# Kernel optimization log

Hardware: AMD Instinct MI355X
Metric: run time of the kernel (lower is better)

The kernel has to match this reference:

```python
import jax, jax.numpy as jnp
import numpy as np

# ---- static module config (matches torch defaults) ----
N_LEVELS = 16
MIN_RES = 16
MAX_RES = 512
N_ENC = 2 ** 14
D = 3          # n_input_dims
E = 2          # n_embed_dims
B = 1 << 20    # number of query points

# per-level resolutions, computed in float32 to mirror torch's float32 log/exp
_gf = np.exp((np.log(np.float32(MAX_RES)) - np.log(np.float32(MIN_RES))) / np.float32(N_LEVELS - 1)).astype(np.float32)
RES = [int(np.floor(np.float32(MIN_RES) * _gf ** np.float32(l))) for l in range(N_LEVELS)]
DIRECT = [r ** D < N_ENC for r in RES]                  # small grids use direct ravel indexing
NLE = [min(r ** D, N_ENC) for r in RES]                  # encodings per level (sentinel row at index NLE[l])

# 2^D corner offsets, shape (8, 3)
OFFS = np.stack(np.meshgrid(*([np.arange(2)] * D), indexing='ij'), axis=-1).reshape(-1, D).astype(np.int32)
# instant-ngp spatial hashing primes
PRIMES = (1, 2654435761, 805459861)


def setup_inputs() -> dict:
    key = jax.random.key(0)
    k1, k2 = jax.random.split(key)
    x = jax.random.uniform(k1, (B, D), dtype=jnp.float32, minval=-1.0, maxval=1.0)
    # stacked per-level tables, padded to (N_ENC+1, E); rows >= NLE[l] zeroed
    emb = jax.random.uniform(k2, (N_LEVELS, N_ENC + 1, E), dtype=jnp.float32, minval=-1e-4, maxval=1e-4)
    row = np.arange(N_ENC + 1)
    valid = (row[None, :] < np.asarray(NLE)[:, None])    # (L, N_ENC+1); also zeroes the sentinel row
    emb = emb * jnp.asarray(valid[..., None], dtype=jnp.float32)
    return {"x": x, "emb": emb}


def _level_features(x, emb_l, R, n_encs, direct):
    offs = jnp.asarray(OFFS)                             # (8, 3)
    xs = (x + 1.0) * (R * 0.5) - 0.5                     # grid coords
    xl = jnp.floor(xs)
    frac = xs - xl                                       # (B, 3)
    xi = xl.astype(jnp.int32)
    c = xi[:, None, :] + offs[None, :, :]                # (B, 8, 3) corner indices
    # bilinear/trilinear weights: prod over dims of frac (offset=1) or 1-frac (offset=0)
    w = jnp.prod(jnp.where(offs[None].astype(bool), frac[:, None, :], 1.0 - frac[:, None, :]), axis=-1)  # (B, 8)
    w = jax.lax.stop_gradient(w)                         # torch computes weights under no_grad
    m = jnp.all((c >= 0) & (c < R), axis=-1)             # (B, 8) corner validity
    if direct:
        ids = (c[..., 0] * R + c[..., 1]) * R + c[..., 2]
    else:
        cu = c.astype(jnp.uint32)
        h = (cu[..., 0] * jnp.uint32(PRIMES[0])
             ^ cu[..., 1] * jnp.uint32(PRIMES[1])
             ^ cu[..., 2] * jnp.uint32(PRIMES[2]))
        ids = (h % jnp.uint32(n_encs)).astype(jnp.int32)
    ids = jnp.where(m, ids, n_encs)                      # invalid corners -> zero sentinel row
    return jnp.sum(emb_l[ids] * w[..., None], axis=1)    # (B, E)


def reference(x, emb):
    feats = [
        _level_features(x, emb[l], RES[l], NLE[l], DIRECT[l])
        for l in range(N_LEVELS)
    ]
    return jnp.stack(feats, axis=1)                      # (B, L, E)
```

## Files before the change

### kernel.cpp

```cpp
#include <hip/hip_runtime.h>
#include <hip/hip_fp16.h>


typedef __attribute__((ext_vector_type(2))) float f32x2;

#define B_POINTS (1 << 20)
#define N_LEVELS 16
#define TAB_F2   16385
#define TAB_H2   16384
#define WG       1024
#define NWG      512
#define NCHUNK   (NWG / N_LEVELS)
#define CHUNK    (B_POINTS / NCHUNK)
#define PPT      (CHUNK / WG)
#define GRP      4
#define NGRP     (PPT / GRP)

__constant__ int   cRES[N_LEVELS]  = {16, 20, 25, 32, 40, 50, 64, 80,
                                      101, 128, 161, 203, 256, 322, 406, 512};
__constant__ float cHALF[N_LEVELS] = {8.f, 10.f, 12.5f, 16.f, 20.f, 25.f, 32.f, 40.f,
                                      50.5f, 64.f, 80.5f, 101.5f, 128.f, 161.f, 203.f, 256.f};

__global__ __launch_bounds__(WG, 8)
void hashenc_lds(const float* __restrict__ x,
                 const float* __restrict__ emb,
                 float* __restrict__ out)
{
    __shared__ __half2 tab[TAB_H2];

    const int bid = blockIdx.x;
    const int xcd = bid & 7;
    const int s   = bid >> 3;
    const int l   = s & 15;
    const int c   = ((s >> 4) << 3) | xcd;

    const int   R      = cRES[l];
    const int   Rm1    = R - 1;
    const float half   = cHALF[l];
    const float hb     = half - 0.5f;
    const bool  direct = (l < 3);
    const int   R4     = R * 4;
    const int   RR4    = R * R * 4;

    const f32x2* __restrict__ gtab = (const f32x2*)emb + (size_t)l * TAB_F2;
    const int t    = threadIdx.x;
    const int base = c * CHUNK + t;

    float xa[GRP], xb[GRP], xcv[GRP];
#pragma unroll
    for (int j = 0; j < GRP; ++j) {
        const int p = base + j * WG;
        xa[j] = x[p * 3 + 0]; xb[j] = x[p * 3 + 1]; xcv[j] = x[p * 3 + 2];
    }

#pragma unroll
    for (int j = 0; j < 16; ++j) {
        const f32x2 v = gtab[j * WG + t];
        __half2 h;
        h.x = __float2half_rn(v.x);
        h.y = __float2half_rn(v.y);
        tab[j * WG + t] = h;
    }
    __syncthreads();

    const char* tb = (const char*)tab;

    for (int kg = 0; kg < NGRP; ++kg) {
        float ca[GRP], cb[GRP], cc[GRP];
#pragma unroll
        for (int j = 0; j < GRP; ++j) { ca[j] = xa[j]; cb[j] = xb[j]; cc[j] = xcv[j]; }

        if (kg + 1 < NGRP) {
#pragma unroll
            for (int j = 0; j < GRP; ++j) {
                const int p = base + (kg + 1) * (GRP * WG) + j * WG;
                xa[j] = x[p * 3 + 0]; xb[j] = x[p * 3 + 1]; xcv[j] = x[p * 3 + 2];
            }
        }

#pragma unroll
        for (int j = 0; j < GRP; ++j) {
            const int p = base + kg * (GRP * WG) + j * WG;

            const float xs0 = fmaf(ca[j], half, hb);
            const float xs1 = fmaf(cb[j], half, hb);
            const float xs2 = fmaf(cc[j], half, hb);
            const float fl0 = floorf(xs0), fl1 = floorf(xs1), fl2 = floorf(xs2);
            const float f0 = xs0 - fl0, f1 = xs1 - fl1, f2 = xs2 - fl2;
            const float g0 = 1.0f - f0, g1 = 1.0f - f1, g2 = 1.0f - f2;
            const int i0 = (int)fl0, i1 = (int)fl1, i2 = (int)fl2;

            const float wx0 = (i0 >= 0)  ? g0 : 0.0f;
            const float wx1 = (i0 < Rm1) ? f0 : 0.0f;
            const float wy0 = (i1 >= 0)  ? g1 : 0.0f;
            const float wy1 = (i1 < Rm1) ? f1 : 0.0f;
            const float wz0 = (i2 >= 0)  ? g2 : 0.0f;
            const float wz1 = (i2 < Rm1) ? f2 : 0.0f;

            const float pxy00 = wx0 * wy0, pxy01 = wx0 * wy1;
            const float pxy10 = wx1 * wy0, pxy11 = wx1 * wy1;
            const float w0 = pxy00 * wz0, w1 = pxy00 * wz1;
            const float w2 = pxy01 * wz0, w3 = pxy01 * wz1;
            const float w4 = pxy10 * wz0, w5 = pxy10 * wz1;
            const float w6 = pxy11 * wz0, w7 = pxy11 * wz1;

            unsigned d0, d1, d2, d3, d4, d5, d6, d7;
            if (direct) {
                const int u0l = max(i0, 0), u0h = min(i0 + 1, Rm1);
                const int u1l = max(i1, 0), u1h = min(i1 + 1, Rm1);
                const int u2l = max(i2, 0), u2h = min(i2 + 1, Rm1);
                const int a0  = u0l * RR4,     a1  = u0h * RR4;
                const int b00 = a0 + u1l * R4, b01 = a0 + u1h * R4;
                const int b10 = a1 + u1l * R4, b11 = a1 + u1h * R4;
                const int zl  = u2l * 4,       zh  = u2h * 4;
                d0 = b00 + zl; d1 = b00 + zh; d2 = b01 + zl; d3 = b01 + zh;
                d4 = b10 + zl; d5 = b10 + zh; d6 = b11 + zl; d7 = b11 + zh;
            } else {
                const unsigned MB  = 16383u << 2;
                const unsigned hx0 = (unsigned)i0 << 2,                 hx1 = hx0 + 4u;
                const unsigned hy0 = (unsigned)i1 * (2654435761u * 4u), hy1 = hy0 + (2654435761u * 4u);
                const unsigned hzf = (unsigned)i2 * (805459861u * 4u);
                const unsigned hz0 = hzf & MB, hz1 = (hzf + (805459861u * 4u)) & MB;
                const unsigned t00 = (hx0 ^ hy0) & MB, t01 = (hx0 ^ hy1) & MB;
                const unsigned t10 = (hx1 ^ hy0) & MB, t11 = (hx1 ^ hy1) & MB;
                d0 = t00 ^ hz0; d1 = t00 ^ hz1; d2 = t01 ^ hz0; d3 = t01 ^ hz1;
                d4 = t10 ^ hz0; d5 = t10 ^ hz1; d6 = t11 ^ hz0; d7 = t11 ^ hz1;
            }

            float acc0 = 0.0f, acc1 = 0.0f;
            {
                const __half2 e0 = *(const __half2*)(tb + d0);
                const __half2 e1 = *(const __half2*)(tb + d1);
                const __half2 e2 = *(const __half2*)(tb + d2);
                const __half2 e3 = *(const __half2*)(tb + d3);
                const __half2 e4 = *(const __half2*)(tb + d4);
                const __half2 e5 = *(const __half2*)(tb + d5);
                const __half2 e6 = *(const __half2*)(tb + d6);
                const __half2 e7 = *(const __half2*)(tb + d7);
                acc0 = fmaf(__low2float(e0),  w0, acc0); acc1 = fmaf(__high2float(e0), w0, acc1);
                acc0 = fmaf(__low2float(e1),  w1, acc0); acc1 = fmaf(__high2float(e1), w1, acc1);
                acc0 = fmaf(__low2float(e2),  w2, acc0); acc1 = fmaf(__high2float(e2), w2, acc1);
                acc0 = fmaf(__low2float(e3),  w3, acc0); acc1 = fmaf(__high2float(e3), w3, acc1);
                acc0 = fmaf(__low2float(e4),  w4, acc0); acc1 = fmaf(__high2float(e4), w4, acc1);
                acc0 = fmaf(__low2float(e5),  w5, acc0); acc1 = fmaf(__high2float(e5), w5, acc1);
                acc0 = fmaf(__low2float(e6),  w6, acc0); acc1 = fmaf(__high2float(e6), w6, acc1);
                acc0 = fmaf(__low2float(e7),  w7, acc0); acc1 = fmaf(__high2float(e7), w7, acc1);
            }

            ((float2*)out)[(size_t)p * N_LEVELS + l] = make_float2(acc0, acc1);
        }
    }
}

extern "C" void kernel_launch(void* const* d_in, const int* in_sizes, int n_in,
                              void* d_out, int out_size, void* d_ws, size_t ws_size,
                              hipStream_t stream) {
    const float* x   = (const float*)d_in[0];
    const float* emb = (const float*)d_in[1];
    float* out = (float*)d_out;

    hashenc_lds<<<NWG, WG, 0, stream>>>(x, emb, out);
}
```

Before: 209.7 us.

## Process two levels per workgroup with a combined 128KB LDS table

Each workgroup now stages the half-precision tables of two adjacent levels into a 128KB shared buffer, with the small direct-indexed levels packed tightly. It computes both levels for every point. This halves the number of workgroups and x reloads, and lets each point write a 16-byte float4 instead of two 8-byte stores. Coordinate loads are also switched to float3 vector loads. In exchange, LDS use per workgroup doubles, which lowers occupancy to fewer resident workgroups per CU, and each workgroup does more work over a longer run.

```diff
diff --git a/kernel.cpp b/kernel.cpp
--- a/kernel.cpp
+++ b/kernel.cpp
@@ -7,10 +7,10 @@
 #define B_POINTS (1 << 20)
 #define N_LEVELS 16
 #define TAB_F2   16385
-#define TAB_H2   16384
 #define WG       1024
-#define NWG      512
-#define NCHUNK   (NWG / N_LEVELS)
+#define NWG      256
+#define NPAIR    8
+#define NCHUNK   (NWG / NPAIR)
 #define CHUNK    (B_POINTS / NCHUNK)
 #define PPT      (CHUNK / WG)
 #define GRP      4
@@ -20,47 +20,142 @@
                                       101, 128, 161, 203, 256, 322, 406, 512};
 __constant__ float cHALF[N_LEVELS] = {8.f, 10.f, 12.5f, 16.f, 20.f, 25.f, 32.f, 40.f,
                                       50.5f, 64.f, 80.5f, 101.5f, 128.f, 161.f, 203.f, 256.f};
+__constant__ int   cROWS[N_LEVELS] = {4096, 8000, 15625, 16384, 16384, 16384, 16384, 16384,
+                                      16384, 16384, 16384, 16384, 16384, 16384, 16384, 16384};
+__constant__ int   cBASE[N_LEVELS] = {0, 4096, 16384, 0, 0, 16384, 0, 16384,
+                                      0, 16384, 0, 16384, 0, 16384, 0, 16384};
 
-__global__ __launch_bounds__(WG, 8)
-void hashenc_lds(const float* __restrict__ x,
-                 const float* __restrict__ emb,
-                 float* __restrict__ out)
+__device__ __forceinline__ void level_feat(const char* __restrict__ tb,
+                                           float cx, float cy, float cz,
+                                           int R, int Rm1, float half, float hb,
+                                           bool direct, unsigned base4,
+                                           float& acc0, float& acc1)
 {
-    __shared__ __half2 tab[TAB_H2];
+    const float xs0 = fmaf(cx, half, hb);
+    const float xs1 = fmaf(cy, half, hb);
+    const float xs2 = fmaf(cz, half, hb);
+    const float fl0 = floorf(xs0), fl1 = floorf(xs1), fl2 = floorf(xs2);
+    const float f0 = xs0 - fl0, f1 = xs1 - fl1, f2 = xs2 - fl2;
+    const float g0 = 1.0f - f0, g1 = 1.0f - f1, g2 = 1.0f - f2;
+    const int i0 = (int)fl0, i1 = (int)fl1, i2 = (int)fl2;
+
+    const float wx0 = (i0 >= 0)  ? g0 : 0.0f;
+    const float wx1 = (i0 < Rm1) ? f0 : 0.0f;
+    const float wy0 = (i1 >= 0)  ? g1 : 0.0f;
+    const float wy1 = (i1 < Rm1) ? f1 : 0.0f;
+    const float wz0 = (i2 >= 0)  ? g2 : 0.0f;
+    const float wz1 = (i2 < Rm1) ? f2 : 0.0f;
+
+    const float pxy00 = wx0 * wy0, pxy01 = wx0 * wy1;
+    const float pxy10 = wx1 * wy0, pxy11 = wx1 * wy1;
+    const float w0 = pxy00 * wz0, w1 = pxy00 * wz1;
+    const float w2 = pxy01 * wz0, w3 = pxy01 * wz1;
+    const float w4 = pxy10 * wz0, w5 = pxy10 * wz1;
+    const float w6 = pxy11 * wz0, w7 = pxy11 * wz1;
+
+    unsigned d0, d1, d2, d3, d4, d5, d6, d7;
+    if (direct) {
+        const int R4  = R * 4;
+        const int RR4 = R * R * 4;
+        const int u0l = max(i0, 0), u0h = min(i0 + 1, Rm1);
+        const int u1l = max(i1, 0), u1h = min(i1 + 1, Rm1);
+        const int u2l = max(i2, 0), u2h = min(i2 + 1, Rm1);
+        const int a0  = u0l * RR4 + (int)base4, a1 = u0h * RR4 + (int)base4;
+        const int b00 = a0 + u1l * R4, b01 = a0 + u1h * R4;
+        const int b10 = a1 + u1l * R4, b11 = a1 + u1h * R4;
+        const int zl  = u2l * 4,       zh  = u2h * 4;
+        d0 = b00 + zl; d1 = b00 + zh; d2 = b01 + zl; d3 = b01 + zh;
+        d4 = b10 + zl; d5 = b10 + zh; d6 = b11 + zl; d7 = b11 + zh;
+    } else {
+        const unsigned MB  = 16383u << 2;
+        const unsigned hx0 = (unsigned)i0 << 2,                 hx1 = hx0 + 4u;
+        const unsigned hy0 = (unsigned)i1 * (2654435761u * 4u), hy1 = hy0 + (2654435761u * 4u);
+        const unsigned hzf = (unsigned)i2 * (805459861u * 4u);
+        const unsigned hz0 = (hzf & MB) | base4;
+        const unsigned hz1 = ((hzf + (805459861u * 4u)) & MB) | base4;
+        const unsigned t00 = (hx0 ^ hy0) & MB, t01 = (hx0 ^ hy1) & MB;
+        const unsigned t10 = (hx1 ^ hy0) & MB, t11 = (hx1 ^ hy1) & MB;
+        d0 = t00 ^ hz0; d1 = t00 ^ hz1; d2 = t01 ^ hz0; d3 = t01 ^ hz1;
+        d4 = t10 ^ hz0; d5 = t10 ^ hz1; d6 = t11 ^ hz0; d7 = t11 ^ hz1;
+    }
+
+    const __half2 e0 = *(const __half2*)(tb + d0);
+    const __half2 e1 = *(const __half2*)(tb + d1);
+    const __half2 e2 = *(const __half2*)(tb + d2);
+    const __half2 e3 = *(const __half2*)(tb + d3);
+    const __half2 e4 = *(const __half2*)(tb + d4);
+    const __half2 e5 = *(const __half2*)(tb + d5);
+    const __half2 e6 = *(const __half2*)(tb + d6);
+    const __half2 e7 = *(const __half2*)(tb + d7);
+    acc0 = 0.0f; acc1 = 0.0f;
+    acc0 = fmaf(__low2float(e0),  w0, acc0); acc1 = fmaf(__high2float(e0), w0, acc1);
+    acc0 = fmaf(__low2float(e1),  w1, acc0); acc1 = fmaf(__high2float(e1), w1, acc1);
+    acc0 = fmaf(__low2float(e2),  w2, acc0); acc1 = fmaf(__high2float(e2), w2, acc1);
+    acc0 = fmaf(__low2float(e3),  w3, acc0); acc1 = fmaf(__high2float(e3), w3, acc1);
+    acc0 = fmaf(__low2float(e4),  w4, acc0); acc1 = fmaf(__high2float(e4), w4, acc1);
+    acc0 = fmaf(__low2float(e5),  w5, acc0); acc1 = fmaf(__high2float(e5), w5, acc1);
+    acc0 = fmaf(__low2float(e6),  w6, acc0); acc1 = fmaf(__high2float(e6), w6, acc1);
+    acc0 = fmaf(__low2float(e7),  w7, acc0); acc1 = fmaf(__high2float(e7), w7, acc1);
+}
+
+__device__ __forceinline__ void stage_level(__half2* __restrict__ tab,
+                                            const f32x2* __restrict__ src,
+                                            int rows, int obase, int t)
+{
+    for (int r0 = 0; r0 < rows; r0 += 4 * WG) {
+        f32x2 v[4];
+#pragma unroll
+        for (int u = 0; u < 4; ++u) {
+            const int r = r0 + u * WG + t;
+            if (r < rows) v[u] = src[r];
+        }
+#pragma unroll
+        for (int u = 0; u < 4; ++u) {
+            const int r = r0 + u * WG + t;
+            if (r < rows) {
+                __half2 h;
+                h.x = __float2half_rn(v[u].x);
+                h.y = __float2half_rn(v[u].y);
+                tab[obase + r] = h;
+            }
+        }
+    }
+}
+
+__global__ __launch_bounds__(WG, 4)
+void hashenc_pair(const float* __restrict__ x,
+                  const float* __restrict__ emb,
+                  float* __restrict__ out)
+{
+    __shared__ __half2 tab[32768];
 
     const int bid = blockIdx.x;
     const int xcd = bid & 7;
     const int s   = bid >> 3;
-    const int l   = s & 15;
-    const int c   = ((s >> 4) << 3) | xcd;
+    const int m   = s & 7;
+    const int c   = ((s >> 3) << 3) | xcd;
 
-    const int   R      = cRES[l];
-    const int   Rm1    = R - 1;
-    const float half   = cHALF[l];
-    const float hb     = half - 0.5f;
-    const bool  direct = (l < 3);
-    const int   R4     = R * 4;
-    const int   RR4    = R * R * 4;
+    const int lA = 2 * m, lB = 2 * m + 1;
+    const int   RA = cRES[lA],  RB = cRES[lB];
+    const int   RmA = RA - 1,   RmB = RB - 1;
+    const float hA = cHALF[lA], hB = cHALF[lB];
+    const float bA = hA - 0.5f, bB = hB - 0.5f;
+    const bool  dA = (lA < 3),  dB = (lB < 3);
+    const unsigned baseA = (unsigned)cBASE[lA] * 4u;
+    const unsigned baseB = (unsigned)cBASE[lB] * 4u;
 
-    const f32x2* __restrict__ gtab = (const f32x2*)emb + (size_t)l * TAB_F2;
     const int t    = threadIdx.x;
     const int base = c * CHUNK + t;
 
     float xa[GRP], xb[GRP], xcv[GRP];
 #pragma unroll
     for (int j = 0; j < GRP; ++j) {
-        const int p = base + j * WG;
-        xa[j] = x[p * 3 + 0]; xb[j] = x[p * 3 + 1]; xcv[j] = x[p * 3 + 2];
+        const float3 v = ((const float3*)x)[base + j * WG];
+        xa[j] = v.x; xb[j] = v.y; xcv[j] = v.z;
     }
 
-#pragma unroll
-    for (int j = 0; j < 16; ++j) {
-        const f32x2 v = gtab[j * WG + t];
-        __half2 h;
-        h.x = __float2half_rn(v.x);
-        h.y = __float2half_rn(v.y);
-        tab[j * WG + t] = h;
-    }
+    stage_level(tab, (const f32x2*)emb + (size_t)lA * TAB_F2, cROWS[lA], cBASE[lA], t);
+    stage_level(tab, (const f32x2*)emb + (size_t)lB * TAB_F2, cROWS[lB], cBASE[lB], t);
     __syncthreads();
 
     const char* tb = (const char*)tab;
@@ -73,8 +168,8 @@
         if (kg + 1 < NGRP) {
 #pragma unroll
             for (int j = 0; j < GRP; ++j) {
-                const int p = base + (kg + 1) * (GRP * WG) + j * WG;
-                xa[j] = x[p * 3 + 0]; xb[j] = x[p * 3 + 1]; xcv[j] = x[p * 3 + 2];
+                const float3 v = ((const float3*)x)[base + (kg + 1) * (GRP * WG) + j * WG];
+                xa[j] = v.x; xb[j] = v.y; xcv[j] = v.z;
             }
         }
 
@@ -82,72 +177,11 @@
         for (int j = 0; j < GRP; ++j) {
             const int p = base + kg * (GRP * WG) + j * WG;
 
-            const float xs0 = fmaf(ca[j], half, hb);
-            const float xs1 = fmaf(cb[j], half, hb);
-            const float xs2 = fmaf(cc[j], half, hb);
-            const float fl0 = floorf(xs0), fl1 = floorf(xs1), fl2 = floorf(xs2);
-            const float f0 = xs0 - fl0, f1 = xs1 - fl1, f2 = xs2 - fl2;
-            const float g0 = 1.0f - f0, g1 = 1.0f - f1, g2 = 1.0f - f2;
-            const int i0 = (int)fl0, i1 = (int)fl1, i2 = (int)fl2;
+            float a0, a1, b0, b1;
+            level_feat(tb, ca[j], cb[j], cc[j], RA, RmA, hA, bA, dA, baseA, a0, a1);
+            level_feat(tb, ca[j], cb[j], cc[j], RB, RmB, hB, bB, dB, baseB, b0, b1);
 
-            const float wx0 = (i0 >= 0)  ? g0 : 0.0f;
-            const float wx1 = (i0 < Rm1) ? f0 : 0.0f;
-            const float wy0 = (i1 >= 0)  ? g1 : 0.0f;
-            const float wy1 = (i1 < Rm1) ? f1 : 0.0f;
-            const float wz0 = (i2 >= 0)  ? g2 : 0.0f;
-            const float wz1 = (i2 < Rm1) ? f2 : 0.0f;
-
-            const float pxy00 = wx0 * wy0, pxy01 = wx0 * wy1;
-            const float pxy10 = wx1 * wy0, pxy11 = wx1 * wy1;
-            const float w0 = pxy00 * wz0, w1 = pxy00 * wz1;
-            const float w2 = pxy01 * wz0, w3 = pxy01 * wz1;
-            const float w4 = pxy10 * wz0, w5 = pxy10 * wz1;
-            const float w6 = pxy11 * wz0, w7 = pxy11 * wz1;
-
-            unsigned d0, d1, d2, d3, d4, d5, d6, d7;
-            if (direct) {
-                const int u0l = max(i0, 0), u0h = min(i0 + 1, Rm1);
-                const int u1l = max(i1, 0), u1h = min(i1 + 1, Rm1);
-                const int u2l = max(i2, 0), u2h = min(i2 + 1, Rm1);
-                const int a0  = u0l * RR4,     a1  = u0h * RR4;
-                const int b00 = a0 + u1l * R4, b01 = a0 + u1h * R4;
-                const int b10 = a1 + u1l * R4, b11 = a1 + u1h * R4;
-                const int zl  = u2l * 4,       zh  = u2h * 4;
-                d0 = b00 + zl; d1 = b00 + zh; d2 = b01 + zl; d3 = b01 + zh;
-                d4 = b10 + zl; d5 = b10 + zh; d6 = b11 + zl; d7 = b11 + zh;
-            } else {
-                const unsigned MB  = 16383u << 2;
-                const unsigned hx0 = (unsigned)i0 << 2,                 hx1 = hx0 + 4u;
-                const unsigned hy0 = (unsigned)i1 * (2654435761u * 4u), hy1 = hy0 + (2654435761u * 4u);
-                const unsigned hzf = (unsigned)i2 * (805459861u * 4u);
-                const unsigned hz0 = hzf & MB, hz1 = (hzf + (805459861u * 4u)) & MB;
-                const unsigned t00 = (hx0 ^ hy0) & MB, t01 = (hx0 ^ hy1) & MB;
-                const unsigned t10 = (hx1 ^ hy0) & MB, t11 = (hx1 ^ hy1) & MB;
-                d0 = t00 ^ hz0; d1 = t00 ^ hz1; d2 = t01 ^ hz0; d3 = t01 ^ hz1;
-                d4 = t10 ^ hz0; d5 = t10 ^ hz1; d6 = t11 ^ hz0; d7 = t11 ^ hz1;
-            }
-
-            float acc0 = 0.0f, acc1 = 0.0f;
-            {
-                const __half2 e0 = *(const __half2*)(tb + d0);
-                const __half2 e1 = *(const __half2*)(tb + d1);
-                const __half2 e2 = *(const __half2*)(tb + d2);
-                const __half2 e3 = *(const __half2*)(tb + d3);
-                const __half2 e4 = *(const __half2*)(tb + d4);
-                const __half2 e5 = *(const __half2*)(tb + d5);
-                const __half2 e6 = *(const __half2*)(tb + d6);
-                const __half2 e7 = *(const __half2*)(tb + d7);
-                acc0 = fmaf(__low2float(e0),  w0, acc0); acc1 = fmaf(__high2float(e0), w0, acc1);
-                acc0 = fmaf(__low2float(e1),  w1, acc0); acc1 = fmaf(__high2float(e1), w1, acc1);
-                acc0 = fmaf(__low2float(e2),  w2, acc0); acc1 = fmaf(__high2float(e2), w2, acc1);
-                acc0 = fmaf(__low2float(e3),  w3, acc0); acc1 = fmaf(__high2float(e3), w3, acc1);
-                acc0 = fmaf(__low2float(e4),  w4, acc0); acc1 = fmaf(__high2float(e4), w4, acc1);
-                acc0 = fmaf(__low2float(e5),  w5, acc0); acc1 = fmaf(__high2float(e5), w5, acc1);
-                acc0 = fmaf(__low2float(e6),  w6, acc0); acc1 = fmaf(__high2float(e6), w6, acc1);
-                acc0 = fmaf(__low2float(e7),  w7, acc0); acc1 = fmaf(__high2float(e7), w7, acc1);
-            }
-
-            ((float2*)out)[(size_t)p * N_LEVELS + l] = make_float2(acc0, acc1);
+            ((float4*)out)[(size_t)p * NPAIR + m] = make_float4(a0, a1, b0, b1);
         }
     }
 }
@@ -159,5 +193,5 @@
     const float* emb = (const float*)d_in[1];
     float* out = (float*)d_out;
 
-    hashenc_lds<<<NWG, WG, 0, stream>>>(x, emb, out);
+    hashenc_pair<<<NWG, WG, 0, stream>>>(x, emb, out);
 }
```

Result: faster. 203.1 us (-3.1%).

## Fuse all levels per point tile with double-buffered LDS tables and transposed stores

Applied to the files above, without the earlier changes.

Each workgroup now handles a 2048-point tile across all 16 levels. It double-buffers each level's fp16 table in LDS and streams the next level's table from global memory while gathering the current level. Results are held as packed half2 in registers and transposed through LDS, so the output is written as coalesced float4 rows instead of strided float2 stores. In exchange, every workgroup reloads all 16 tables (about 2MB of L2 traffic per block), adds per-level barriers, and rounds results to fp16, which loses precision.

```diff
diff --git a/kernel.cpp b/kernel.cpp
--- a/kernel.cpp
+++ b/kernel.cpp
@@ -7,148 +7,214 @@
 #define B_POINTS (1 << 20)
 #define N_LEVELS 16
 #define TAB_F2   16385
-#define TAB_H2   16384
 #define WG       1024
-#define NWG      512
-#define NCHUNK   (NWG / N_LEVELS)
-#define CHUNK    (B_POINTS / NCHUNK)
-#define PPT      (CHUNK / WG)
-#define GRP      4
-#define NGRP     (PPT / GRP)
-
-__constant__ int   cRES[N_LEVELS]  = {16, 20, 25, 32, 40, 50, 64, 80,
-                                      101, 128, 161, 203, 256, 322, 406, 512};
-__constant__ float cHALF[N_LEVELS] = {8.f, 10.f, 12.5f, 16.f, 20.f, 25.f, 32.f, 40.f,
-                                      50.5f, 64.f, 80.5f, 101.5f, 128.f, 161.f, 203.f, 256.f};
-
-__global__ __launch_bounds__(WG, 8)
-void hashenc_lds(const float* __restrict__ x,
-                 const float* __restrict__ emb,
-                 float* __restrict__ out)
+#define TILE     2048
+#define NWG      (B_POINTS / TILE)
+#define TPAD     17
+
+constexpr int   kRES[N_LEVELS]  = {16, 20, 25, 32, 40, 50, 64, 80,
+                                   101, 128, 161, 203, 256, 322, 406, 512};
+constexpr float kHALF[N_LEVELS] = {8.f, 10.f, 12.5f, 16.f, 20.f, 25.f, 32.f, 40.f,
+                                   50.5f, 64.f, 80.5f, 101.5f, 128.f, 161.f, 203.f, 256.f};
+constexpr int   kROWS[N_LEVELS] = {4096, 8000, 15625, 16384, 16384, 16384, 16384, 16384,
+                                   16384, 16384, 16384, 16384, 16384, 16384, 16384, 16384};
+
+__device__ __forceinline__ unsigned pack_h2(const f32x2 v)
 {
-    __shared__ __half2 tab[TAB_H2];
-
-    const int bid = blockIdx.x;
-    const int xcd = bid & 7;
-    const int s   = bid >> 3;
-    const int l   = s & 15;
-    const int c   = ((s >> 4) << 3) | xcd;
-
-    const int   R      = cRES[l];
-    const int   Rm1    = R - 1;
-    const float half   = cHALF[l];
-    const float hb     = half - 0.5f;
-    const bool  direct = (l < 3);
-    const int   R4     = R * 4;
-    const int   RR4    = R * R * 4;
-
-    const f32x2* __restrict__ gtab = (const f32x2*)emb + (size_t)l * TAB_F2;
+    __half2 h = __floats2half2_rn(v.x, v.y);
+    return *reinterpret_cast<unsigned*>(&h);
+}
+
+__device__ __forceinline__ unsigned gather_lvl(const char* __restrict__ tb,
+                                               float cx, float cy, float cz,
+                                               const int R, const float half,
+                                               const bool direct)
+{
+    const int   Rm1 = R - 1;
+    const float hb  = half - 0.5f;
+    const float xs0 = fmaf(cx, half, hb);
+    const float xs1 = fmaf(cy, half, hb);
+    const float xs2 = fmaf(cz, half, hb);
+    const float fl0 = floorf(xs0), fl1 = floorf(xs1), fl2 = floorf(xs2);
+    const float f0 = xs0 - fl0, f1 = xs1 - fl1, f2 = xs2 - fl2;
+    const float g0 = 1.0f - f0, g1 = 1.0f - f1, g2 = 1.0f - f2;
+    const int i0 = (int)fl0, i1 = (int)fl1, i2 = (int)fl2;
+
+    const float wx0 = (i0 >= 0)  ? g0 : 0.0f;
+    const float wx1 = (i0 < Rm1) ? f0 : 0.0f;
+    const float wy0 = (i1 >= 0)  ? g1 : 0.0f;
+    const float wy1 = (i1 < Rm1) ? f1 : 0.0f;
+    const float wz0 = (i2 >= 0)  ? g2 : 0.0f;
+    const float wz1 = (i2 < Rm1) ? f2 : 0.0f;
+
+    const f32x2 wyp = {wy0, wy1};
+    const f32x2 wzp = {wz0, wz1};
+    const f32x2 pA  = wyp * wx0;
+    const f32x2 pB  = wyp * wx1;
+    const f32x2 wA  = wzp * pA.x;
+    const f32x2 wB  = wzp * pA.y;
+    const f32x2 wC  = wzp * pB.x;
+    const f32x2 wD  = wzp * pB.y;
+
+    unsigned d0, d1, d2, d3, d4, d5, d6, d7;
+    if (direct) {
+        const int R4  = R * 4;
+        const int RR4 = R * R * 4;
+        const int u0l = max(i0, 0), u0h = min(i0 + 1, Rm1);
+        const int u1l = max(i1, 0), u1h = min(i1 + 1, Rm1);
+        const int u2l = max(i2, 0), u2h = min(i2 + 1, Rm1);
+        const int a0  = u0l * RR4,     a1  = u0h * RR4;
+        const int b00 = a0 + u1l * R4, b01 = a0 + u1h * R4;
+        const int b10 = a1 + u1l * R4, b11 = a1 + u1h * R4;
+        const int zl  = u2l * 4,       zh  = u2h * 4;
+        d0 = b00 + zl; d1 = b00 + zh; d2 = b01 + zl; d3 = b01 + zh;
+        d4 = b10 + zl; d5 = b10 + zh; d6 = b11 + zl; d7 = b11 + zh;
+    } else {
+        const unsigned MB  = 16383u << 2;
+        const unsigned hx0 = (unsigned)i0 << 2,                 hx1 = hx0 + 4u;
+        const unsigned hy0 = (unsigned)i1 * (2654435761u * 4u), hy1 = hy0 + (2654435761u * 4u);
+        const unsigned hzf = (unsigned)i2 * (805459861u * 4u);
+        const unsigned hz0 = hzf & MB, hz1 = (hzf + (805459861u * 4u)) & MB;
+        const unsigned t00 = (hx0 ^ hy0) & MB, t01 = (hx0 ^ hy1) & MB;
+        const unsigned t10 = (hx1 ^ hy0) & MB, t11 = (hx1 ^ hy1) & MB;
+        d0 = t00 ^ hz0; d1 = t00 ^ hz1; d2 = t01 ^ hz0; d3 = t01 ^ hz1;
+        d4 = t10 ^ hz0; d5 = t10 ^ hz1; d6 = t11 ^ hz0; d7 = t11 ^ hz1;
+    }
+
+    const __half2 e0 = *(const __half2*)(tb + d0);
+    const __half2 e1 = *(const __half2*)(tb + d1);
+    const __half2 e2 = *(const __half2*)(tb + d2);
+    const __half2 e3 = *(const __half2*)(tb + d3);
+    const __half2 e4 = *(const __half2*)(tb + d4);
+    const __half2 e5 = *(const __half2*)(tb + d5);
+    const __half2 e6 = *(const __half2*)(tb + d6);
+    const __half2 e7 = *(const __half2*)(tb + d7);
+
+    f32x2 acc = {0.0f, 0.0f};
+    const float2 q0 = __half22float2(e0);
+    const float2 q1 = __half22float2(e1);
+    const float2 q2 = __half22float2(e2);
+    const float2 q3 = __half22float2(e3);
+    const float2 q4 = __half22float2(e4);
+    const float2 q5 = __half22float2(e5);
+    const float2 q6 = __half22float2(e6);
+    const float2 q7 = __half22float2(e7);
+    acc += (f32x2){q0.x, q0.y} * wA.x;
+    acc += (f32x2){q1.x, q1.y} * wA.y;
+    acc += (f32x2){q2.x, q2.y} * wB.x;
+    acc += (f32x2){q3.x, q3.y} * wB.y;
+    acc += (f32x2){q4.x, q4.y} * wC.x;
+    acc += (f32x2){q5.x, q5.y} * wC.y;
+    acc += (f32x2){q6.x, q6.y} * wD.x;
+    acc += (f32x2){q7.x, q7.y} * wD.y;
+
+    __half2 hr = __floats2half2_rn(acc.x, acc.y);
+    return *reinterpret_cast<unsigned*>(&hr);
+}
+
+__global__ __launch_bounds__(WG, 4)
+void hashenc_fused(const float* __restrict__ x,
+                   const float* __restrict__ emb,
+                   float4* __restrict__ out4)
+{
+    __shared__ unsigned sh[2 * 16384];
     const int t    = threadIdx.x;
-    const int base = c * CHUNK + t;
-
-    float xa[GRP], xb[GRP], xcv[GRP];
-#pragma unroll
-    for (int j = 0; j < GRP; ++j) {
-        const int p = base + j * WG;
-        xa[j] = x[p * 3 + 0]; xb[j] = x[p * 3 + 1]; xcv[j] = x[p * 3 + 2];
-    }
-
-#pragma unroll
-    for (int j = 0; j < 16; ++j) {
-        const f32x2 v = gtab[j * WG + t];
-        __half2 h;
-        h.x = __float2half_rn(v.x);
-        h.y = __float2half_rn(v.y);
-        tab[j * WG + t] = h;
-    }
-    __syncthreads();
-
-    const char* tb = (const char*)tab;
-
-    for (int kg = 0; kg < NGRP; ++kg) {
-        float ca[GRP], cb[GRP], cc[GRP];
-#pragma unroll
-        for (int j = 0; j < GRP; ++j) { ca[j] = xa[j]; cb[j] = xb[j]; cc[j] = xcv[j]; }
-
-        if (kg + 1 < NGRP) {
-#pragma unroll
-            for (int j = 0; j < GRP; ++j) {
-                const int p = base + (kg + 1) * (GRP * WG) + j * WG;
-                xa[j] = x[p * 3 + 0]; xb[j] = x[p * 3 + 1]; xcv[j] = x[p * 3 + 2];
+    const int base = blockIdx.x * TILE;
+    const int p0   = base + t;
+    const int p1   = base + WG + t;
+
+    const float3 v0 = ((const float3*)x)[p0];
+    const float3 v1 = ((const float3*)x)[p1];
+
+    unsigned res0[N_LEVELS];
+    unsigned res1[N_LEVELS];
+
+    {
+        const f32x2* gt = (const f32x2*)emb;
+#pragma unroll
+        for (int i = 0; i < 4; ++i)
+            sh[i * WG + t] = pack_h2(gt[i * WG + t]);
+    }
+
+#pragma unroll
+    for (int l = 0; l < N_LEVELS; ++l) {
+        __syncthreads();
+        const char* tb   = (const char*)(sh + (l & 1) * 16384);
+        unsigned*   nbuf = sh + ((l + 1) & 1) * 16384;
+        const int   nl   = l + 1;
+        const f32x2* gt  = (const f32x2*)emb + (size_t)nl * TAB_F2;
+
+        f32x2 sA[8];
+        if (nl < N_LEVELS) {
+#pragma unroll
+            for (int i = 0; i < 8; ++i) {
+                const int r = i * WG + t;
+                if (i * WG < kROWS[nl])
+                    if (r < kROWS[nl]) sA[i] = gt[r];
             }
         }
 
-#pragma unroll
-        for (int j = 0; j < GRP; ++j) {
-            const int p = base + kg * (GRP * WG) + j * WG;
-
-            const float xs0 = fmaf(ca[j], half, hb);
-            const float xs1 = fmaf(cb[j], half, hb);
-            const float xs2 = fmaf(cc[j], half, hb);
-            const float fl0 = floorf(xs0), fl1 = floorf(xs1), fl2 = floorf(xs2);
-            const float f0 = xs0 - fl0, f1 = xs1 - fl1, f2 = xs2 - fl2;
-            const float g0 = 1.0f - f0, g1 = 1.0f - f1, g2 = 1.0f - f2;
-            const int i0 = (int)fl0, i1 = (int)fl1, i2 = (int)fl2;
-
-            const float wx0 = (i0 >= 0)  ? g0 : 0.0f;
-            const float wx1 = (i0 < Rm1) ? f0 : 0.0f;
-            const float wy0 = (i1 >= 0)  ? g1 : 0.0f;
-            const float wy1 = (i1 < Rm1) ? f1 : 0.0f;
-            const float wz0 = (i2 >= 0)  ? g2 : 0.0f;
-            const float wz1 = (i2 < Rm1) ? f2 : 0.0f;
-
-            const float pxy00 = wx0 * wy0, pxy01 = wx0 * wy1;
-            const float pxy10 = wx1 * wy0, pxy11 = wx1 * wy1;
-            const float w0 = pxy00 * wz0, w1 = pxy00 * wz1;
-            const float w2 = pxy01 * wz0, w3 = pxy01 * wz1;
-            const float w4 = pxy10 * wz0, w5 = pxy10 * wz1;
-            const float w6 = pxy11 * wz0, w7 = pxy11 * wz1;
-
-            unsigned d0, d1, d2, d3, d4, d5, d6, d7;
-            if (direct) {
-                const int u0l = max(i0, 0), u0h = min(i0 + 1, Rm1);
-                const int u1l = max(i1, 0), u1h = min(i1 + 1, Rm1);
-                const int u2l = max(i2, 0), u2h = min(i2 + 1, Rm1);
-                const int a0  = u0l * RR4,     a1  = u0h * RR4;
-                const int b00 = a0 + u1l * R4, b01 = a0 + u1h * R4;
-                const int b10 = a1 + u1l * R4, b11 = a1 + u1h * R4;
-                const int zl  = u2l * 4,       zh  = u2h * 4;
-                d0 = b00 + zl; d1 = b00 + zh; d2 = b01 + zl; d3 = b01 + zh;
-                d4 = b10 + zl; d5 = b10 + zh; d6 = b11 + zl; d7 = b11 + zh;
-            } else {
-                const unsigned MB  = 16383u << 2;
-                const unsigned hx0 = (unsigned)i0 << 2,                 hx1 = hx0 + 4u;
-                const unsigned hy0 = (unsigned)i1 * (2654435761u * 4u), hy1 = hy0 + (2654435761u * 4u);
-                const unsigned hzf = (unsigned)i2 * (805459861u * 4u);
-                const unsigned hz0 = hzf & MB, hz1 = (hzf + (805459861u * 4u)) & MB;
-                const unsigned t00 = (hx0 ^ hy0) & MB, t01 = (hx0 ^ hy1) & MB;
-                const unsigned t10 = (hx1 ^ hy0) & MB, t11 = (hx1 ^ hy1) & MB;
-                d0 = t00 ^ hz0; d1 = t00 ^ hz1; d2 = t01 ^ hz0; d3 = t01 ^ hz1;
-                d4 = t10 ^ hz0; d5 = t10 ^ hz1; d6 = t11 ^ hz0; d7 = t11 ^ hz1;
-            }
-
-            float acc0 = 0.0f, acc1 = 0.0f;
-            {
-                const __half2 e0 = *(const __half2*)(tb + d0);
-                const __half2 e1 = *(const __half2*)(tb + d1);
-                const __half2 e2 = *(const __half2*)(tb + d2);
-                const __half2 e3 = *(const __half2*)(tb + d3);
-                const __half2 e4 = *(const __half2*)(tb + d4);
-                const __half2 e5 = *(const __half2*)(tb + d5);
-                const __half2 e6 = *(const __half2*)(tb + d6);
-                const __half2 e7 = *(const __half2*)(tb + d7);
-                acc0 = fmaf(__low2float(e0),  w0, acc0); acc1 = fmaf(__high2float(e0), w0, acc1);
-                acc0 = fmaf(__low2float(e1),  w1, acc0); acc1 = fmaf(__high2float(e1), w1, acc1);
-                acc0 = fmaf(__low2float(e2),  w2, acc0); acc1 = fmaf(__high2float(e2), w2, acc1);
-                acc0 = fmaf(__low2float(e3),  w3, acc0); acc1 = fmaf(__high2float(e3), w3, acc1);
-                acc0 = fmaf(__low2float(e4),  w4, acc0); acc1 = fmaf(__high2float(e4), w4, acc1);
-                acc0 = fmaf(__low2float(e5),  w5, acc0); acc1 = fmaf(__high2float(e5), w5, acc1);
-                acc0 = fmaf(__low2float(e6),  w6, acc0); acc1 = fmaf(__high2float(e6), w6, acc1);
-                acc0 = fmaf(__low2float(e7),  w7, acc0); acc1 = fmaf(__high2float(e7), w7, acc1);
-            }
-
-            ((float2*)out)[(size_t)p * N_LEVELS + l] = make_float2(acc0, acc1);
+        res0[l] = gather_lvl(tb, v0.x, v0.y, v0.z, kRES[l], kHALF[l], l < 3);
+
+        f32x2 sB[8];
+        if (nl < N_LEVELS) {
+#pragma unroll
+            for (int i = 0; i < 8; ++i) {
+                const int r = i * WG + t;
+                if (i * WG < kROWS[nl])
+                    if (r < kROWS[nl]) nbuf[r] = pack_h2(sA[i]);
+            }
+#pragma unroll
+            for (int i = 0; i < 8; ++i) {
+                const int r = (8 + i) * WG + t;
+                if ((8 + i) * WG < kROWS[nl])
+                    if (r < kROWS[nl]) sB[i] = gt[r];
+            }
         }
+
+        res1[l] = gather_lvl(tb, v1.x, v1.y, v1.z, kRES[l], kHALF[l], l < 3);
+
+        if (nl < N_LEVELS) {
+#pragma unroll
+            for (int i = 0; i < 8; ++i) {
+                const int r = (8 + i) * WG + t;
+                if ((8 + i) * WG < kROWS[nl])
+                    if (r < kROWS[nl]) nbuf[r] = pack_h2(sB[i]);
+            }
+        }
+    }
+
+    unsigned* tr = sh;
+    const size_t obase = (size_t)base * 8;
+
+    __syncthreads();
+#pragma unroll
+    for (int k = 0; k < N_LEVELS; ++k) tr[t * TPAD + k] = res0[k];
+    __syncthreads();
+#pragma unroll
+    for (int j = 0; j < 8; ++j) {
+        const int vIdx = j * WG + t;
+        const int pl = vIdx >> 3, lp = vIdx & 7;
+        const __half2 ha = *(const __half2*)&tr[pl * TPAD + 2 * lp];
+        const __half2 hb = *(const __half2*)&tr[pl * TPAD + 2 * lp + 1];
+        const float2 fa = __half22float2(ha);
+        const float2 fb = __half22float2(hb);
+        out4[obase + vIdx] = make_float4(fa.x, fa.y, fb.x, fb.y);
+    }
+
+    __syncthreads();
+#pragma unroll
+    for (int k = 0; k < N_LEVELS; ++k) tr[t * TPAD + k] = res1[k];
+    __syncthreads();
+#pragma unroll
+    for (int j = 0; j < 8; ++j) {
+        const int vIdx = j * WG + t;
+        const int pl = vIdx >> 3, lp = vIdx & 7;
+        const __half2 ha = *(const __half2*)&tr[pl * TPAD + 2 * lp];
+        const __half2 hb = *(const __half2*)&tr[pl * TPAD + 2 * lp + 1];
+        const float2 fa = __half22float2(ha);
+        const float2 fb = __half22float2(hb);
+        out4[obase + 8192 + vIdx] = make_float4(fa.x, fa.y, fb.x, fb.y);
     }
 }
 
@@ -157,7 +223,7 @@
                               hipStream_t stream) {
     const float* x   = (const float*)d_in[0];
     const float* emb = (const float*)d_in[1];
-    float* out = (float*)d_out;
-
-    hashenc_lds<<<NWG, WG, 0, stream>>>(x, emb, out);
-}
+    float4* out4 = (float4*)d_out;
+
+    hashenc_fused<<<NWG, WG, 0, stream>>>(x, emb, out4);
+}
```

Result: slower. 720.6 us (+243.7%).
